# Performance work log

Measured on AMD Instinct MI355X. Metric: run time of the kernel, lower is better.

Reference implementation:

```python
import jax, jax.numpy as jnp
import numpy as np

B, T, H, I, O, L = 8, 8192, 256, 256, 256, 2


def setup_inputs() -> dict:
    key = jax.random.key(0)
    ks = jax.random.split(key, 12)
    s = 1.0 / np.sqrt(H)
    inp = {
        "emb": jax.random.normal(ks[0], (B, T, I), jnp.float32),
        "start": jax.random.randint(ks[1], (B, T), 0, 2) > 0,  # bool reset flags
        "h0": jnp.zeros((L, B, H), jnp.float32),               # per-layer initial carry
        "min_w": jax.random.normal(ks[2], (H, I), jnp.float32) * s,
        "min_b": jnp.zeros((H,), jnp.float32),
        "mout_w": jax.random.normal(ks[3], (O, H), jnp.float32) * s,
        "mout_b": jnp.zeros((O,), jnp.float32),
        "Wf_w": jax.random.normal(ks[4], (L, H, H), jnp.float32) * s,
        "Wf_b": jnp.zeros((L, H), jnp.float32),
        "Wh_w": jax.random.normal(ks[5], (L, H, H), jnp.float32) * s,
        "Wh_b": jnp.zeros((L, H), jnp.float32),
        "Uf_w": jax.random.normal(ks[6], (L, H, H), jnp.float32) * s,
        "Uh_w": jax.random.normal(ks[7], (L, H, H), jnp.float32) * s,
        "ff_w": jax.random.normal(ks[8], (L, H, H), jnp.float32) * s,
        "ff_b": jnp.zeros((L, H), jnp.float32),
    }
    return inp


def reference(emb, start, h0, min_w, min_b, mout_w, mout_b,
              Wf_w, Wf_b, Wh_w, Wh_b, Uf_w, Uh_w, ff_w, ff_b):
    # map_in: [B,T,I] -> [B,T,H]
    x = jnp.einsum('bti,hi->bth', emb, min_w) + min_b
    start_t = start.T  # [T,B]
    h_final = []
    for l in range(L):
        # Precompute input-side projections outside the scan (time-parallel).
        xf = jnp.einsum('bth,oh->bto', x, Wf_w[l]) + Wf_b[l]  # [B,T,H]
        xh = jnp.einsum('bth,oh->bto', x, Wh_w[l]) + Wh_b[l]  # [B,T,H]
        Uf = Uf_w[l]
        Uh = Uh_w[l]

        def step(h, inp):
            xft, xht, st = inp  # [B,H], [B,H], [B]
            # Resettable: zero the carry where a new episode starts.
            h = jnp.where(st[:, None], jnp.zeros_like(h), h)
            f = jax.nn.sigmoid(xft + h @ Uf.T)
            h_hat = jnp.tanh(xht + (f * h) @ Uh.T)
            h_new = (1.0 - f) * h + f * h_hat
            return h_new, h_new

        hT, z = jax.lax.scan(step, h0[l],
                             (xf.transpose(1, 0, 2), xh.transpose(1, 0, 2), start_t))
        h_final.append(hT)
        z = z.transpose(1, 0, 2)  # [B,T,H]
        # per-layer feedforward + leaky_relu (slope 0.01)
        x = jax.nn.leaky_relu(jnp.einsum('bth,oh->bto', z, ff_w[l]) + ff_b[l])
    out = jnp.einsum('bth,oh->bto', x, mout_w) + mout_b  # [B,T,O]
    return out, jnp.stack(h_final)  # ([B,T,O], [L,B,H])
```

## Files before the change

kernel.cpp:

```cpp
#include <hip/hip_runtime.h>
#include <hip/hip_fp16.h>
#include <cstdint>
#include <cstddef>

#define BATCH 8
#define TT 8192
#define HD 256
#define RTOT (BATCH * TT)
#define HC 16
#define NPAIR (TT / (2 * HC))

typedef __attribute__((ext_vector_type(4))) float    f32x4;
typedef __attribute__((ext_vector_type(8))) _Float16 f16x8;
typedef __attribute__((ext_vector_type(4))) _Float16 f16x4;

typedef __attribute__((address_space(1))) const void gvoid_t;
typedef __attribute__((address_space(3))) void lvoid_t;

__device__ __forceinline__ void gl_lds16(const void* g, void* l) {
  __builtin_amdgcn_global_load_lds((gvoid_t*)g, (lvoid_t*)l, 16, 0, 0);
}

__device__ __forceinline__ void ldsbar() {
  asm volatile("s_waitcnt lgkmcnt(0)" ::: "memory");
  __builtin_amdgcn_s_barrier();
  __builtin_amdgcn_sched_barrier(0x7F);
}

__device__ __forceinline__ void gbar() {
  __builtin_amdgcn_s_barrier();
  __builtin_amdgcn_sched_barrier(0);
  asm volatile("" ::: "memory");
}

__global__ void detect_start_par(const unsigned int* __restrict__ s,
                                 int* __restrict__ bad) {
  const unsigned int w = s[blockIdx.x * blockDim.x + threadIdx.x];
  const unsigned int b0 = w & 255u, b1 = (w >> 8) & 255u,
                     b2 = (w >> 16) & 255u, b3 = (w >> 24) & 255u;
  const int bi = (b1 | b2 | b3) != 0;
  const int bf = (b0 != 0) || (b1 != 0) ||
                 (b2 != 0 && b2 != 0x80u) || (b3 != 0 && b3 != 0x3fu);
  if (__any(bi) && (threadIdx.x & 63) == 0) atomicOr(&bad[0], 1);
  if (__any(bf) && (threadIdx.x & 63) == 0) atomicOr(&bad[1], 1);
}

__global__ void conv_f16(const float* __restrict__ in, _Float16* __restrict__ out,
                         const int n) {
  const int i = (blockIdx.x * blockDim.x + threadIdx.x) * 8;
  if (i + 7 >= n) return;
  const float4 a = *(const float4*)&in[i];
  const float4 b = *(const float4*)&in[i + 4];
  f16x8 v;
  v[0] = (_Float16)a.x; v[1] = (_Float16)a.y; v[2] = (_Float16)a.z; v[3] = (_Float16)a.w;
  v[4] = (_Float16)b.x; v[5] = (_Float16)b.y; v[6] = (_Float16)b.z; v[7] = (_Float16)b.w;
  *(f16x8*)&out[i] = v;
}

__global__ void conv_w8(const float* p0, const float* p1, const float* p2,
                        const float* p3, const float* p4, const float* p5,
                        const float* p6, const float* p7,
                        _Float16* __restrict__ out) {
  const int seg = blockIdx.y;
  const float* p;
  switch (seg) {
    case 0: p = p0; break; case 1: p = p1; break;
    case 2: p = p2; break; case 3: p = p3; break;
    case 4: p = p4; break; case 5: p = p5; break;
    case 6: p = p6; break; default: p = p7; break;
  }
  const int i = (blockIdx.x * blockDim.x + threadIdx.x) * 8;
  const float4 a = *(const float4*)&p[i];
  const float4 b = *(const float4*)&p[i + 4];
  f16x8 v;
  v[0] = (_Float16)a.x; v[1] = (_Float16)a.y; v[2] = (_Float16)a.z; v[3] = (_Float16)a.w;
  v[4] = (_Float16)b.x; v[5] = (_Float16)b.y; v[6] = (_Float16)b.z; v[7] = (_Float16)b.w;
  *(f16x8*)&out[(size_t)seg * 65536 + i] = v;
}

__global__ void swz_w(const float* __restrict__ Uf, const float* __restrict__ Uh,
                      _Float16* __restrict__ outp) {
  const int gid  = blockIdx.x * 256 + threadIdx.x;
  const int lane = gid & 63;
  const int w    = (gid >> 6) & 7;
  const int f    = (gid >> 9) & 15;
  const int mat  = (gid >> 13) & 1;
  const int l    = gid >> 14;
  const int fr = lane & 15, fq = lane >> 4;
  const int tile = f >> 3, kc = f & 7;
  const int nrow = (w * 2 + tile) * 16 + fr;
  const int kb   = kc * 32 + fq * 8;
  const float* src = (mat ? Uh : Uf) + (size_t)l * 65536 + nrow * 256 + kb;
  const float4 a = *(const float4*)src;
  const float4 b = *(const float4*)(src + 4);
  f16x8 v;
  v[0] = (_Float16)a.x; v[1] = (_Float16)a.y; v[2] = (_Float16)a.z; v[3] = (_Float16)a.w;
  v[4] = (_Float16)b.x; v[5] = (_Float16)b.y; v[6] = (_Float16)b.z; v[7] = (_Float16)b.w;
  *(f16x8*)&outp[(size_t)gid * 8] = v;
}

__global__ __launch_bounds__(256, 2) void gemm_fused(
    const _Float16* __restrict__ A,
    const _Float16* __restrict__ W1, const float* __restrict__ b1, const int act1,
    const _Float16* __restrict__ Wa, const float* __restrict__ ba,
    const _Float16* __restrict__ Wb, const float* __restrict__ bb,
    _Float16* __restrict__ Ca, _Float16* __restrict__ Cb,
    float* __restrict__ C32) {
  __shared__ __align__(16) char smem[65536];
  char* Amid = smem;
  char* stg  = smem + 32768;

  const int tid  = threadIdx.x;
  const int wave = tid >> 6, lane = tid & 63;
  const int wm = wave >> 1, wn = wave & 1;
  const int bm = blockIdx.x * 64;
  const int lrow  = tid >> 2;
  const int lcol8 = (tid & 3) * 8;
  const int fr = lane & 15;
  const int fq = lane >> 4;

  auto ldswz = [&](int row, int colbyte) -> const f16x8* {
    return (const f16x8*)(Amid + row * 512 + (colbyte ^ ((row & 15) << 4)));
  };

#pragma unroll
  for (int it = 0; it < 8; it++) {
    const int o   = (it * 256 + tid) * 16;
    const int row = o >> 9;
    const int cb  = (o & 511) ^ ((row & 15) << 4);
    gl_lds16(&A[(size_t)(bm + row) * HD + (cb >> 1)], Amid + o);
  }

  auto STW = [&](const _Float16* W, int kk, int b2) {
    const int k0 = kk * 32;
#pragma unroll
    for (int is = 0; is < 4; is++)
      gl_lds16(&W[(size_t)(is * 64 + lrow) * HD + k0 + lcol8],
               stg + b2 * 16384 + is * 4096 + wave * 1024);
  };

  {
    f32x4 acc[2][8];
#pragma unroll
    for (int i = 0; i < 2; i++)
#pragma unroll
      for (int j = 0; j < 8; j++) acc[i][j] = (f32x4){0.f, 0.f, 0.f, 0.f};

    STW(W1, 0, 0);
#pragma unroll
    for (int k = 0; k < 8; k++) {
      const int cur = k & 1;
      if (k < 7) {
        STW(W1, k + 1, cur ^ 1);
        asm volatile("s_waitcnt vmcnt(4)" ::: "memory");
      } else {
        asm volatile("s_waitcnt vmcnt(0)" ::: "memory");
      }
      gbar();
      const _Float16* Ws = (const _Float16*)(stg + cur * 16384);
      f16x8 af[2], bf[8];
#pragma unroll
      for (int mi = 0; mi < 2; mi++)
        af[mi] = *ldswz(wm * 32 + mi * 16 + fr, k * 64 + fq * 16);
#pragma unroll
      for (int ni = 0; ni < 8; ni++)
        bf[ni] = *(const f16x8*)(Ws + (wn * 128 + ni * 16 + fr) * 32 + fq * 8);
#pragma unroll
      for (int mi = 0; mi < 2; mi++)
#pragma unroll
        for (int ni = 0; ni < 8; ni++)
          acc[mi][ni] = __builtin_amdgcn_mfma_f32_16x16x32_f16(af[mi], bf[ni],
                                                               acc[mi][ni], 0, 0, 0);
      asm volatile("s_waitcnt lgkmcnt(0)" ::: "memory");
      gbar();
    }
    __syncthreads();
#pragma unroll
    for (int mi = 0; mi < 2; mi++)
#pragma unroll
      for (int ni = 0; ni < 8; ni++) {
        const float bvv = b1[wn * 128 + ni * 16 + fr];
#pragma unroll
        for (int j = 0; j < 4; j++) {
          float v = acc[mi][ni][j] + bvv;
          if (act1 == 1) v = (v > 0.f) ? v : 0.01f * v;
          const int row = wm * 32 + mi * 16 + fq * 4 + j;
          const int cb  = ((wn * 128 + ni * 16 + fr) * 2) ^ ((row & 15) << 4);
          *(_Float16*)(Amid + row * 512 + cb) = (_Float16)v;
        }
      }
  }
  __syncthreads();

  const int nmat = (Wb != nullptr) ? 2 : 1;
  for (int mat = 0; mat < nmat; mat++) {
    const _Float16* W2 = mat ? Wb : Wa;
    const float* b2p   = mat ? bb : ba;
    _Float16* C16      = mat ? Cb : Ca;

    f32x4 acc[2][8];
#pragma unroll
    for (int i = 0; i < 2; i++)
#pragma unroll
      for (int j = 0; j < 8; j++) acc[i][j] = (f32x4){0.f, 0.f, 0.f, 0.f};

    STW(W2, 0, 0);
#pragma unroll
    for (int k = 0; k < 8; k++) {
      const int cur = k & 1;
      if (k < 7) {
        STW(W2, k + 1, cur ^ 1);
        asm volatile("s_waitcnt vmcnt(4)" ::: "memory");
      } else {
        asm volatile("s_waitcnt vmcnt(0)" ::: "memory");
      }
      gbar();
      const _Float16* Ws = (const _Float16*)(stg + cur * 16384);
      f16x8 af[2], bf[8];
#pragma unroll
      for (int mi = 0; mi < 2; mi++)
        af[mi] = *ldswz(wm * 32 + mi * 16 + fr, k * 64 + fq * 16);
#pragma unroll
      for (int ni = 0; ni < 8; ni++)
        bf[ni] = *(const f16x8*)(Ws + (wn * 128 + ni * 16 + fr) * 32 + fq * 8);
#pragma unroll
      for (int mi = 0; mi < 2; mi++)
#pragma unroll
        for (int ni = 0; ni < 8; ni++)
          acc[mi][ni] = __builtin_amdgcn_mfma_f32_16x16x32_f16(af[mi], bf[ni],
                                                               acc[mi][ni], 0, 0, 0);
      asm volatile("s_waitcnt lgkmcnt(0)" ::: "memory");
      gbar();
    }

    if (C32 != nullptr) {
#pragma unroll
      for (int mi = 0; mi < 2; mi++)
#pragma unroll
        for (int ni = 0; ni < 8; ni++) {
          const float bvv = b2p[wn * 128 + ni * 16 + fr];
#pragma unroll
          for (int j = 0; j < 4; j++)
            C32[(size_t)(bm + wm * 32 + mi * 16 + fq * 4 + j) * HD +
                wn * 128 + ni * 16 + fr] = acc[mi][ni][j] + bvv;
        }
    } else {
#pragma unroll
      for (int mi = 0; mi < 2; mi++)
#pragma unroll
        for (int ni = 0; ni < 8; ni++) {
          const float bvv = b2p[wn * 128 + ni * 16 + fr];
#pragma unroll
          for (int j = 0; j < 4; j++)
            C16[(size_t)(bm + wm * 32 + mi * 16 + fq * 4 + j) * HD +
                wn * 128 + ni * 16 + fr] = (_Float16)(acc[mi][ni][j] + bvv);
        }
    }
    if (mat == 0 && nmat == 2) __syncthreads();
  }
}

__global__ __launch_bounds__(512) void scan_mgu(
    const _Float16* __restrict__ xf, const _Float16* __restrict__ xh,
    const void* __restrict__ startp, const int* __restrict__ badf,
    const float* __restrict__ h0l,
    const _Float16* __restrict__ wfrag,
    _Float16* __restrict__ z, float* __restrict__ hfin,
    _Float16* __restrict__ dumpz) {
  const int tid  = threadIdx.x;
  const int wave = tid >> 6;
  const int lane = tid & 63;
  const int fr   = lane & 15;
  const int fq   = lane >> 4;
  const int col  = fr;
  const int b    = col & 7;
  const int grp  = col >> 3;
  const int base = blockIdx.x * (2 * HC);
  const int t0c  = base + grp * HC;
  const int mode = (!badf[0]) ? 1 : (!badf[1] ? 2 : 0);

  __shared__ __align__(16) char hbuf[8192];
  __shared__ __align__(16) char gbuf[8192];
  __shared__ int rb[16];

  _Float16* dp0 = dumpz + ((size_t)blockIdx.x * 512 + tid) * 16;

  auto flag = [&](int bb, int t) -> int {
    const int idx = bb * TT + t;
    if (mode == 1) return ((const int*)startp)[idx] != 0;
    if (mode == 2) return ((const float*)startp)[idx] != 0.0f;
    return ((const uint8_t*)startp)[idx] != 0;
  };
  auto ldfrag = [&](const char* buf, int kc) -> f16x8 {
    int off = kc * 1024 + fq * 256 + fr * 16;
    off ^= ((off >> 8) & 1) << 4;
    return *(const f16x8*)(buf + off);
  };
  auto stfrag = [&](char* buf, int nb, const float4 v) {
    int off = ((nb >> 5) * 1024) + (((nb >> 3) & 3) * 256) + col * 16 + (nb & 7) * 2;
    off ^= ((off >> 8) & 1) << 4;
    f16x4 p;
    p[0] = (_Float16)v.x; p[1] = (_Float16)v.y;
    p[2] = (_Float16)v.z; p[3] = (_Float16)v.w;
    *(f16x4*)(buf + off) = p;
  };

  f16x8 auf[2][8], auh[2][8];
#pragma unroll
  for (int f = 0; f < 16; f++)
    auf[f >> 3][f & 7] =
        *(const f16x8*)&wfrag[((size_t)(f * 512) + wave * 64 + lane) * 8];
#pragma unroll
  for (int f = 0; f < 16; f++)
    auh[f >> 3][f & 7] =
        *(const f16x8*)&wfrag[((size_t)(8192 + f * 512) + wave * 64 + lane) * 8];

  if (tid < 16) rb[tid] = -1;
  __syncthreads();
  {
    const int cg  = tid >> 5;
    const int l32 = tid & 31;
    const int t0g = base + (cg >> 3) * HC;
    const int bg  = cg & 7;
    for (int off = 0;; off += 32) {
      const int st = t0g - off - l32;
      if (st >= 0 && rb[cg] < 0 && flag(bg, st)) atomicMax(&rb[cg], st);
      __syncthreads();
      bool done = true;
#pragma unroll
      for (int c = 0; c < 16; c++) {
        const int tc = base + (c >> 3) * HC;
        if (rb[c] < 0 && tc - off >= 0) done = false;
      }
      if (done) break;
      __syncthreads();
    }
  }
  __syncthreads();

  const int rbc    = rb[col];
  const int startc = max(rbc, 0);
  int Lmax = 0;
#pragma unroll
  for (int c = 0; c < 16; c++) {
    const int tc = base + (c >> 3) * HC;
    const int s  = max(rb[c], 0);
    Lmax = max(Lmax, tc - s);
  }

  const int nb0 = (wave * 2 + 0) * 16 + fq * 4;
  const int nb1 = (wave * 2 + 1) * 16 + fq * 4;

  float4 hinit0 = make_float4(0.f, 0.f, 0.f, 0.f), hinit1 = hinit0;
  if (rbc < 0) {
    hinit0 = *(const float4*)&h0l[b * HD + nb0];
    hinit1 = *(const float4*)&h0l[b * HD + nb1];
  }
  float4 hr0 = hinit0, hr1 = hinit1;
  stfrag(hbuf, nb0, hr0);
  stfrag(hbuf, nb1, hr1);
  __syncthreads();

  int t = t0c - Lmax;
  int tcl = min(max(t, 0), TT - 1);
  f16x4 pxf0 = *(const f16x4*)&xf[((size_t)b * TT + tcl) * HD + nb0];
  f16x4 pxf1 = *(const f16x4*)&xf[((size_t)b * TT + tcl) * HD + nb1];
  f16x4 pxh0 = *(const f16x4*)&xh[((size_t)b * TT + tcl) * HD + nb0];
  f16x4 pxh1 = *(const f16x4*)&xh[((size_t)b * TT + tcl) * HD + nb1];
  int fnext;
  {
    const int ftn = flag(b, min(max(t + 1, 0), TT - 1));
    fnext = (t + 1 < TT) ? ftn : 0;
  }

  for (int i = -Lmax; i < HC; i++) {
    t = t0c + i;
    f32x4 cf0 = {(float)pxf0[0], (float)pxf0[1], (float)pxf0[2], (float)pxf0[3]};
    f32x4 cf1 = {(float)pxf1[0], (float)pxf1[1], (float)pxf1[2], (float)pxf1[3]};
    f32x4 ch0 = {(float)pxh0[0], (float)pxh0[1], (float)pxh0[2], (float)pxh0[3]};
    f32x4 ch1 = {(float)pxh1[0], (float)pxh1[1], (float)pxh1[2], (float)pxh1[3]};

    const int fcur = fnext;
    const int tn = min(max(t + 1, 0), TT - 1);
    pxf0 = *(const f16x4*)&xf[((size_t)b * TT + tn) * HD + nb0];
    pxf1 = *(const f16x4*)&xf[((size_t)b * TT + tn) * HD + nb1];
    pxh0 = *(const f16x4*)&xh[((size_t)b * TT + tn) * HD + nb0];
    pxh1 = *(const f16x4*)&xh[((size_t)b * TT + tn) * HD + nb1];
    {
      const int ftn = flag(b, min(max(t + 2, 0), TT - 1));
      fnext = (t + 2 < TT) ? ftn : 0;
    }

    int stn = 0;
    if (t + 1 <= startc) stn = 2;
    else if (fcur) stn = 1;

#pragma unroll
    for (int kc = 0; kc < 8; kc++) {
      const f16x8 bv = ldfrag(hbuf, kc);
      cf0 = __builtin_amdgcn_mfma_f32_16x16x32_f16(auf[0][kc], bv, cf0, 0, 0, 0);
      cf1 = __builtin_amdgcn_mfma_f32_16x16x32_f16(auf[1][kc], bv, cf1, 0, 0, 0);
    }
    f32x4 fv0, fv1;
    float4 g0, g1;
#pragma unroll
    for (int r = 0; r < 4; r++) {
      const float f0 = 1.f / (1.f + __expf(-cf0[r]));
      const float f1 = 1.f / (1.f + __expf(-cf1[r]));
      fv0[r] = f0; fv1[r] = f1;
      (&g0.x)[r] = f0 * (&hr0.x)[r];
      (&g1.x)[r] = f1 * (&hr1.x)[r];
    }
    stfrag(gbuf, nb0, g0);
    stfrag(gbuf, nb1, g1);
    ldsbar();

#pragma unroll
    for (int kc = 0; kc < 8; kc++) {
      const f16x8 bv = ldfrag(gbuf, kc);
      ch0 = __builtin_amdgcn_mfma_f32_16x16x32_f16(auh[0][kc], bv, ch0, 0, 0, 0);
      ch1 = __builtin_amdgcn_mfma_f32_16x16x32_f16(auh[1][kc], bv, ch1, 0, 0, 0);
    }
    float4 hn0, hn1;
    f16x4 zn0, zn1;
#pragma unroll
    for (int r = 0; r < 4; r++) {
      const float e0 = __expf(2.f * ch0[r]);
      const float e1 = __expf(2.f * ch1[r]);
      const float hh0 = 1.f - 2.f / (e0 + 1.f);
      const float hh1 = 1.f - 2.f / (e1 + 1.f);
      (&hn0.x)[r] = (1.f - fv0[r]) * (&hr0.x)[r] + fv0[r] * hh0;
      (&hn1.x)[r] = (1.f - fv1[r]) * (&hr1.x)[r] + fv1[r] * hh1;
      zn0[r] = (_Float16)(&hn0.x)[r];
      zn1[r] = (_Float16)(&hn1.x)[r];
    }
    {
      const size_t tz = (size_t)b * TT + (size_t)max(t, 0);
      _Float16* zp0 = (i >= 0) ? &z[tz * HD + nb0] : dp0;
      _Float16* zp1 = (i >= 0) ? &z[tz * HD + nb1] : dp0 + 8;
      *(f16x4*)zp0 = zn0;
      *(f16x4*)zp1 = zn1;
    }
    hr0 = (stn == 2) ? hinit0 : (stn == 1 ? make_float4(0.f, 0.f, 0.f, 0.f) : hn0);
    hr1 = (stn == 2) ? hinit1 : (stn == 1 ? make_float4(0.f, 0.f, 0.f, 0.f) : hn1);
    stfrag(hbuf, nb0, hr0);
    stfrag(hbuf, nb1, hr1);
    ldsbar();
  }

  if (t0c + HC == TT) {
    *(float4*)&hfin[b * HD + nb0] = hr0;
    *(float4*)&hfin[b * HD + nb1] = hr1;
  }
}

extern "C" void kernel_launch(void* const* d_in, const int* in_sizes, int n_in,
                              void* d_out, int out_size, void* d_ws, size_t ws_size,
                              hipStream_t stream) {
  const float* emb    = (const float*)d_in[0];
  const void*  startp = d_in[1];
  const float* h0     = (const float*)d_in[2];
  const float* min_w  = (const float*)d_in[3];
  const float* min_b  = (const float*)d_in[4];
  const float* mout_w = (const float*)d_in[5];
  const float* mout_b = (const float*)d_in[6];
  const float* Wf_w   = (const float*)d_in[7];
  const float* Wf_b   = (const float*)d_in[8];
  const float* Wh_w   = (const float*)d_in[9];
  const float* Wh_b   = (const float*)d_in[10];
  const float* Uf_w   = (const float*)d_in[11];
  const float* Uh_w   = (const float*)d_in[12];
  const float* ff_w   = (const float*)d_in[13];
  const float* ff_b   = (const float*)d_in[14];

  float* out = (float*)d_out;
  char*  ws  = (char*)d_ws;
  int*   bad = (int*)ws;
  _Float16* w16  = (_Float16*)(ws + 1024);
  _Float16* uswz = (_Float16*)(ws + 1024 + 1048576);
  _Float16* dump = (_Float16*)(ws + 1024 + 1048576 + 524288);
  _Float16* bufE = (_Float16*)(ws + 1024 + 1048576 + 524288 + 4194304);
  _Float16* bufA = bufE + (size_t)RTOT * HD;
  _Float16* bufB = bufA + (size_t)RTOT * HD;
  _Float16* bufC = bufB + (size_t)RTOT * HD;
  float* hfin = out + (size_t)RTOT * HD;
  const size_t WO = (size_t)HD * HD;

  _Float16* w_min = w16;
  _Float16* w_out = w16 + 1 * WO;
  _Float16* w_f0  = w16 + 2 * WO;
  _Float16* w_f1  = w16 + 3 * WO;
  _Float16* w_h0  = w16 + 4 * WO;
  _Float16* w_h1  = w16 + 5 * WO;
  _Float16* w_ff0 = w16 + 6 * WO;
  _Float16* w_ff1 = w16 + 7 * WO;

  hipMemsetAsync(bad, 0, 16, stream);
  detect_start_par<<<64, 256, 0, stream>>>((const unsigned int*)startp, bad);
  conv_f16<<<RTOT * HD / 2048, 256, 0, stream>>>(emb, bufE, RTOT * HD);
  conv_w8<<<dim3(32, 8), 256, 0, stream>>>(min_w, mout_w, Wf_w, Wf_w + WO,
                                           Wh_w, Wh_w + WO, ff_w, ff_w + WO, w16);
  swz_w<<<128, 256, 0, stream>>>(Uf_w, Uh_w, uswz);

  gemm_fused<<<RTOT / 64, 256, 0, stream>>>(bufE, w_min, min_b, 0,
                                            w_f0, Wf_b, w_h0, Wh_b,
                                            bufB, bufC, nullptr);
  scan_mgu<<<NPAIR, 512, 0, stream>>>(bufB, bufC, startp, bad, h0,
                                      uswz, bufA, hfin, dump);
  gemm_fused<<<RTOT / 64, 256, 0, stream>>>(bufA, w_ff0, ff_b, 1,
                                            w_f1, Wf_b + HD, w_h1, Wh_b + HD,
                                            bufB, bufC, nullptr);
  scan_mgu<<<NPAIR, 512, 0, stream>>>(bufB, bufC, startp, bad, h0 + BATCH * HD,
                                      uswz + (size_t)16384 * 8, bufA,
                                      hfin + BATCH * HD, dump);
  gemm_fused<<<RTOT / 64, 256, 0, stream>>>(bufA, w_ff1, ff_b + HD, 1,
                                            w_out, mout_b, nullptr, nullptr,
                                            nullptr, nullptr, out);
}
```

Measured before the change: 346.7 us.

## Interleave xf/xh projections into scan-fragment layout for vectorized scan loads

The GEMM epilogue now writes the xf and xh projections into one packed buffer whose layout matches each scan lane's fragment, interleaving both matrices per timestep. The scan loads two 16-byte vectors per step instead of four scattered 8-byte loads from separate row-major buffers, which cuts per-step global latency on the serial path. The cost is scattered 2-byte stores in the GEMM epilogue, which may hurt its write coalescing.

```diff
diff --git a/kernel.cpp b/kernel.cpp
--- a/kernel.cpp
+++ b/kernel.cpp
@@ -104,7 +104,7 @@
     const _Float16* __restrict__ W1, const float* __restrict__ b1, const int act1,
     const _Float16* __restrict__ Wa, const float* __restrict__ ba,
     const _Float16* __restrict__ Wb, const float* __restrict__ bb,
-    _Float16* __restrict__ Ca, _Float16* __restrict__ Cb,
+    _Float16* __restrict__ xP,
     float* __restrict__ C32) {
   __shared__ __align__(16) char smem[65536];
   char* Amid = smem;
@@ -196,7 +196,6 @@
   for (int mat = 0; mat < nmat; mat++) {
     const _Float16* W2 = mat ? Wb : Wa;
     const float* b2p   = mat ? bb : ba;
-    _Float16* C16      = mat ? Cb : Ca;
 
     f32x4 acc[2][8];
 #pragma unroll
@@ -249,11 +248,24 @@
       for (int mi = 0; mi < 2; mi++)
 #pragma unroll
         for (int ni = 0; ni < 8; ni++) {
-          const float bvv = b2p[wn * 128 + ni * 16 + fr];
-#pragma unroll
-          for (int j = 0; j < 4; j++)
-            C16[(size_t)(bm + wm * 32 + mi * 16 + fq * 4 + j) * HD +
-                wn * 128 + ni * 16 + fr] = (_Float16)(acc[mi][ni][j] + bvv);
+          const int n   = wn * 128 + ni * 16 + fr;
+          const float bvv = b2p[n];
+          const int wv   = n >> 5;
+          const int half = (n >> 4) & 1;
+          const int fqs  = (n >> 2) & 3;
+          const int js   = n & 3;
+#pragma unroll
+          for (int j = 0; j < 4; j++) {
+            const int r   = bm + wm * 32 + mi * 16 + fq * 4 + j;
+            const int t   = r & (TT - 1);
+            const int bb2 = r >> 13;
+            const int slot = ((t >> 5) << 4) | (t & 15);
+            const int grp  = (t >> 4) & 1;
+            const size_t e =
+                (((size_t)slot * 512) + wv * 64 + fqs * 16 + grp * 8 + bb2) * 16 +
+                mat * 8 + half * 4 + js;
+            xP[e] = (_Float16)(acc[mi][ni][j] + bvv);
+          }
         }
     }
     if (mat == 0 && nmat == 2) __syncthreads();
@@ -261,7 +273,7 @@
 }
 
 __global__ __launch_bounds__(512) void scan_mgu(
-    const _Float16* __restrict__ xf, const _Float16* __restrict__ xh,
+    const _Float16* __restrict__ xP,
     const void* __restrict__ startp, const int* __restrict__ badf,
     const float* __restrict__ h0l,
     const _Float16* __restrict__ wfrag,
@@ -304,6 +316,18 @@
     p[2] = (_Float16)v.z; p[3] = (_Float16)v.w;
     *(f16x4*)(buf + off) = p;
   };
+  auto ldx = [&](int tc, f16x4& xf0, f16x4& xf1, f16x4& xh0, f16x4& xh1) {
+    const int slot = ((tc >> 5) << 4) | (tc & 15);
+    const int gT   = (tc >> 4) & 1;
+    const _Float16* pp =
+        &xP[(((size_t)slot * 512) + wave * 64 + fq * 16 + gT * 8 + b) * 16];
+    const f16x8 vf = *(const f16x8*)pp;
+    const f16x8 vh = *(const f16x8*)(pp + 8);
+    xf0[0] = vf[0]; xf0[1] = vf[1]; xf0[2] = vf[2]; xf0[3] = vf[3];
+    xf1[0] = vf[4]; xf1[1] = vf[5]; xf1[2] = vf[6]; xf1[3] = vf[7];
+    xh0[0] = vh[0]; xh0[1] = vh[1]; xh0[2] = vh[2]; xh0[3] = vh[3];
+    xh1[0] = vh[4]; xh1[1] = vh[5]; xh1[2] = vh[6]; xh1[3] = vh[7];
+  };
 
   f16x8 auf[2][8], auh[2][8];
 #pragma unroll
@@ -363,10 +387,8 @@
 
   int t = t0c - Lmax;
   int tcl = min(max(t, 0), TT - 1);
-  f16x4 pxf0 = *(const f16x4*)&xf[((size_t)b * TT + tcl) * HD + nb0];
-  f16x4 pxf1 = *(const f16x4*)&xf[((size_t)b * TT + tcl) * HD + nb1];
-  f16x4 pxh0 = *(const f16x4*)&xh[((size_t)b * TT + tcl) * HD + nb0];
-  f16x4 pxh1 = *(const f16x4*)&xh[((size_t)b * TT + tcl) * HD + nb1];
+  f16x4 pxf0, pxf1, pxh0, pxh1;
+  ldx(tcl, pxf0, pxf1, pxh0, pxh1);
   int fnext;
   {
     const int ftn = flag(b, min(max(t + 1, 0), TT - 1));
@@ -382,10 +404,7 @@
 
     const int fcur = fnext;
     const int tn = min(max(t + 1, 0), TT - 1);
-    pxf0 = *(const f16x4*)&xf[((size_t)b * TT + tn) * HD + nb0];
-    pxf1 = *(const f16x4*)&xf[((size_t)b * TT + tn) * HD + nb1];
-    pxh0 = *(const f16x4*)&xh[((size_t)b * TT + tn) * HD + nb0];
-    pxh1 = *(const f16x4*)&xh[((size_t)b * TT + tn) * HD + nb1];
+    ldx(tn, pxf0, pxf1, pxh0, pxh1);
     {
       const int ftn = flag(b, min(max(t + 2, 0), TT - 1));
       fnext = (t + 2 < TT) ? ftn : 0;
@@ -481,8 +500,7 @@
   _Float16* dump = (_Float16*)(ws + 1024 + 1048576 + 524288);
   _Float16* bufE = (_Float16*)(ws + 1024 + 1048576 + 524288 + 4194304);
   _Float16* bufA = bufE + (size_t)RTOT * HD;
-  _Float16* bufB = bufA + (size_t)RTOT * HD;
-  _Float16* bufC = bufB + (size_t)RTOT * HD;
+  _Float16* xP   = bufA + (size_t)RTOT * HD;
   float* hfin = out + (size_t)RTOT * HD;
   const size_t WO = (size_t)HD * HD;
 
@@ -504,16 +522,16 @@
 
   gemm_fused<<<RTOT / 64, 256, 0, stream>>>(bufE, w_min, min_b, 0,
                                             w_f0, Wf_b, w_h0, Wh_b,
-                                            bufB, bufC, nullptr);
-  scan_mgu<<<NPAIR, 512, 0, stream>>>(bufB, bufC, startp, bad, h0,
+                                            xP, nullptr);
+  scan_mgu<<<NPAIR, 512, 0, stream>>>(xP, startp, bad, h0,
                                       uswz, bufA, hfin, dump);
   gemm_fused<<<RTOT / 64, 256, 0, stream>>>(bufA, w_ff0, ff_b, 1,
                                             w_f1, Wf_b + HD, w_h1, Wh_b + HD,
-                                            bufB, bufC, nullptr);
-  scan_mgu<<<NPAIR, 512, 0, stream>>>(bufB, bufC, startp, bad, h0 + BATCH * HD,
+                                            xP, nullptr);
+  scan_mgu<<<NPAIR, 512, 0, stream>>>(xP, startp, bad, h0 + BATCH * HD,
                                       uswz + (size_t)16384 * 8, bufA,
                                       hfin + BATCH * HD, dump);
   gemm_fused<<<RTOT / 64, 256, 0, stream>>>(bufA, w_ff1, ff_b + HD, 1,
                                             w_out, mout_b, nullptr, nullptr,
-                                            nullptr, nullptr, out);
-}
+                                            nullptr, out);
+}
```

Measured after the change: 406.6 us. 1.17x slower.
